# Kernel optimization log

Hardware: AMD Instinct MI355X
Metric: run time of the kernel (lower is better)

Reference implementation:

```python
import jax, jax.numpy as jnp
import numpy as np

TOPK = 8
N_GROUPS = 8
TOPK_GROUPS = 4
ROUTE_SCALE = 2.5


def setup_inputs() -> dict:
    key = jax.random.key(0)
    k1, k2, k3 = jax.random.split(key, 3)
    T, D, E = 8192, 7168, 256
    x = jax.random.normal(k1, (T, D), dtype=jnp.float32)
    weight = jax.random.normal(k2, (E, D), dtype=jnp.float32) * 0.02
    bias = jax.random.normal(k3, (E,), dtype=jnp.float32) * 0.01
    return {"x": x, "weight": weight, "bias": bias}


def reference(x, weight, bias):
    T = x.shape[0]
    E = weight.shape[0]
    # gate GEMM in fp32 (x.float() @ weight.float().T) + sigmoid scoring
    scores = jax.nn.sigmoid(jnp.einsum('td,ed->te', x, weight))  # [T, E]
    original_scores = scores
    s = scores + bias  # bias only affects routing decisions, not weights
    # group-limited routing: [T, n_groups, experts_per_group]
    sg = s.reshape(T, N_GROUPS, E // N_GROUPS)
    # bias branch: group score = sum of top-2 expert scores within group
    group_scores = jax.lax.top_k(sg, 2)[0].sum(axis=-1)  # [T, G]
    gidx = jax.lax.top_k(group_scores, TOPK_GROUPS)[1]   # [T, topk_groups]
    keep = jnp.zeros((T, N_GROUPS), dtype=bool).at[
        jnp.arange(T)[:, None], gidx].set(True)
    masked = jnp.where(keep[:, :, None], sg, -jnp.inf).reshape(T, E)
    indices = jax.lax.top_k(masked, TOPK)[1]  # [T, topk]
    weights = jnp.take_along_axis(original_scores, indices, axis=1)
    weights = weights / weights.sum(axis=-1, keepdims=True)  # sigmoid norm
    weights = weights * ROUTE_SCALE
    return weights, indices
```

## Files before the change

### kernel.cpp

```cpp
#include <hip/hip_runtime.h>
#include <math.h>

#define T_TOK 8192
#define D_DIM 7168
#define E_EXP 256
#define TOPKN 8
#define NGRP 8
#define TOPG 4
#define ROUTE_SCALEF 2.5f

#define BM 128
#define BK 32

typedef _Float16 f16;
typedef f16 f16x8 __attribute__((ext_vector_type(8)));
typedef float f32x4 __attribute__((ext_vector_type(4)));

__global__ __launch_bounds__(256)
void split_w(const float* __restrict__ W, f16* __restrict__ Wh, f16* __restrict__ Wl) {
  const int e  = blockIdx.x;
  const int se = (e >> 1) & 3;
  for (int s = threadIdx.x; s < D_DIM / 8; s += 256) {
    const int t = s >> 2, c = s & 3;
    const int kin  = t * 32 + ((c ^ se) << 3);
    const int kout = t * 32 + (c << 3);
    const float4 v0 = *(const float4*)(W + (size_t)e * D_DIM + kin);
    const float4 v1 = *(const float4*)(W + (size_t)e * D_DIM + kin + 4);
    const float pe[8] = {v0.x, v0.y, v0.z, v0.w, v1.x, v1.y, v1.z, v1.w};
    f16x8 h, l;
#pragma unroll
    for (int m = 0; m < 8; ++m) {
      const float hf = (float)(f16)pe[m];
      h[m] = (f16)(hf * 64.0f);
      l[m] = (f16)((pe[m] - hf) * 64.0f);
    }
    *(f16x8*)(Wh + (size_t)e * D_DIM + kout) = h;
    *(f16x8*)(Wl + (size_t)e * D_DIM + kout) = l;
  }
}

__device__ __forceinline__ void gload_lds16(const void* g, void* l) {
  __builtin_amdgcn_global_load_lds(
      (const __attribute__((address_space(1))) unsigned int*)g,
      (__attribute__((address_space(3))) unsigned int*)l, 16, 0, 0);
}

__global__ __launch_bounds__(512, 4)
void gate_gemm(const float* __restrict__ X, const f16* __restrict__ Wh,
               const f16* __restrict__ Wl, float* __restrict__ partial, int kper) {
  __shared__ f16 Ah[BM][BK], Al[BM][BK];
  __shared__ f16 Bh[E_EXP][BK], Bl[E_EXP][BK];

  const int tid   = threadIdx.x;
  const int lane  = tid & 63;
  const int wid   = tid >> 6;
  const int mb    = blockIdx.x;
  const int ks    = blockIdx.y;
  const int kbase = ks * kper;
  const int ntile = kper >> 5;

  const int sr = wid * 16 + (lane & 15);
  const int sc = lane >> 4;
  const float* Xp = X + (size_t)(mb * BM + sr) * D_DIM + kbase + (sc << 3);
  const int awoff = ((sc ^ ((sr >> 1) & 3)) << 3);

  const f16* Whp = Wh + (size_t)(wid * 32 + (lane >> 2)) * D_DIM + kbase + ((lane & 3) << 3);
  const f16* Wlp = Wl + (size_t)(wid * 32 + (lane >> 2)) * D_DIM + kbase + ((lane & 3) << 3);

  const int wm0 = (wid >> 2) * 64;
  const int wn0 = (wid & 3) * 64;
  const int fr  = lane & 15;
  const int rdoff = (((lane >> 4) << 3)) ^ (((fr >> 1) & 3) << 3);

  f32x4 acc[4][4];
#pragma unroll
  for (int i = 0; i < 4; ++i)
#pragma unroll
    for (int j = 0; j < 4; ++j) acc[i][j] = f32x4{0.f, 0.f, 0.f, 0.f};

  float4 pa0 = *(const float4*)(Xp);
  float4 pa1 = *(const float4*)(Xp + 4);

#pragma unroll 1
  for (int kt = 0; kt < ntile; ++kt) {
    const int kc = kt << 5;

    gload_lds16(Whp + kc,                      &Bh[wid * 32][0]);
    gload_lds16(Whp + kc + (size_t)16 * D_DIM, &Bh[wid * 32 + 16][0]);
    gload_lds16(Wlp + kc,                      &Bl[wid * 32][0]);
    gload_lds16(Wlp + kc + (size_t)16 * D_DIM, &Bl[wid * 32 + 16][0]);

    const int knext = (kt + 1 < ntile) ? kc + 32 : kc;
    const float4 na0 = *(const float4*)(Xp + knext);
    const float4 na1 = *(const float4*)(Xp + knext + 4);

    const float pe[8] = {pa0.x, pa0.y, pa0.z, pa0.w, pa1.x, pa1.y, pa1.z, pa1.w};
    f16x8 hv, lv;
#pragma unroll
    for (int m = 0; m < 8; ++m) {
      const float hf = (float)(f16)pe[m];
      hv[m] = (f16)(hf * 64.0f);
      lv[m] = (f16)((pe[m] - hf) * 64.0f);
    }
    *(f16x8*)&Ah[sr][awoff] = hv;
    *(f16x8*)&Al[sr][awoff] = lv;
    pa0 = na0; pa1 = na1;

    __syncthreads();

    f16x8 bh0 = *(const f16x8*)&Bh[wn0 +  0 + fr][rdoff];
    f16x8 bl0 = *(const f16x8*)&Bl[wn0 +  0 + fr][rdoff];
    f16x8 bh1 = *(const f16x8*)&Bh[wn0 + 16 + fr][rdoff];
    f16x8 bl1 = *(const f16x8*)&Bl[wn0 + 16 + fr][rdoff];
    f16x8 bh2 = *(const f16x8*)&Bh[wn0 + 32 + fr][rdoff];
    f16x8 bl2 = *(const f16x8*)&Bl[wn0 + 32 + fr][rdoff];
    f16x8 bh3 = *(const f16x8*)&Bh[wn0 + 48 + fr][rdoff];
    f16x8 bl3 = *(const f16x8*)&Bl[wn0 + 48 + fr][rdoff];
#pragma unroll
    for (int i = 0; i < 4; ++i) {
      const f16x8 ah = *(const f16x8*)&Ah[wm0 + i * 16 + fr][rdoff];
      const f16x8 al = *(const f16x8*)&Al[wm0 + i * 16 + fr][rdoff];
      acc[i][0] = __builtin_amdgcn_mfma_f32_16x16x32_f16(ah, bh0, acc[i][0], 0, 0, 0);
      acc[i][0] = __builtin_amdgcn_mfma_f32_16x16x32_f16(ah, bl0, acc[i][0], 0, 0, 0);
      acc[i][0] = __builtin_amdgcn_mfma_f32_16x16x32_f16(al, bh0, acc[i][0], 0, 0, 0);
      acc[i][1] = __builtin_amdgcn_mfma_f32_16x16x32_f16(ah, bh1, acc[i][1], 0, 0, 0);
      acc[i][1] = __builtin_amdgcn_mfma_f32_16x16x32_f16(ah, bl1, acc[i][1], 0, 0, 0);
      acc[i][1] = __builtin_amdgcn_mfma_f32_16x16x32_f16(al, bh1, acc[i][1], 0, 0, 0);
      acc[i][2] = __builtin_amdgcn_mfma_f32_16x16x32_f16(ah, bh2, acc[i][2], 0, 0, 0);
      acc[i][2] = __builtin_amdgcn_mfma_f32_16x16x32_f16(ah, bl2, acc[i][2], 0, 0, 0);
      acc[i][2] = __builtin_amdgcn_mfma_f32_16x16x32_f16(al, bh2, acc[i][2], 0, 0, 0);
      acc[i][3] = __builtin_amdgcn_mfma_f32_16x16x32_f16(ah, bh3, acc[i][3], 0, 0, 0);
      acc[i][3] = __builtin_amdgcn_mfma_f32_16x16x32_f16(ah, bl3, acc[i][3], 0, 0, 0);
      acc[i][3] = __builtin_amdgcn_mfma_f32_16x16x32_f16(al, bh3, acc[i][3], 0, 0, 0);
    }
    __syncthreads();
  }

  const float s = 1.0f / 4096.0f;
  float* pout = partial + (size_t)ks * T_TOK * E_EXP;
#pragma unroll
  for (int i = 0; i < 4; ++i) {
    const int row0 = mb * BM + wm0 + i * 16 + (lane >> 4) * 4;
#pragma unroll
    for (int j = 0; j < 4; ++j) {
      const int col = wn0 + j * 16 + fr;
      const f32x4 v = acc[i][j] * s;
#pragma unroll
      for (int r = 0; r < 4; ++r)
        pout[(size_t)(row0 + r) * E_EXP + col] = v[r];
    }
  }
}

__global__ __launch_bounds__(256)
void gate_route(const float* __restrict__ partial, const float* __restrict__ bias,
                float* __restrict__ wout, float* __restrict__ iout, int ksplit) {
  const int t    = (blockIdx.x * 256 + threadIdx.x) >> 6;
  const int lane = threadIdx.x & 63;

  float sx = 0.f, sy = 0.f, sz = 0.f, sw = 0.f;
  for (int ks = 0; ks < ksplit; ++ks) {
    const float4 p = *(const float4*)(partial + ((size_t)ks * T_TOK + t) * E_EXP + (lane << 2));
    sx += p.x; sy += p.y; sz += p.z; sw += p.w;
  }
  const float o0 = 1.f / (1.f + expf(-sx));
  const float o1 = 1.f / (1.f + expf(-sy));
  const float o2 = 1.f / (1.f + expf(-sz));
  const float o3 = 1.f / (1.f + expf(-sw));
  const float4 bv4 = *(const float4*)(bias + (lane << 2));
  const float b0 = o0 + bv4.x, b1 = o1 + bv4.y, b2 = o2 + bv4.z, b3 = o3 + bv4.w;

  const float ma = fmaxf(b0, b1), mi = fminf(b0, b1);
  const float mb_ = fmaxf(b2, b3), mn = fminf(b2, b3);
  float m1 = fmaxf(ma, mb_);
  float m2 = fmaxf(fminf(ma, mb_), fmaxf(mi, mn));
#pragma unroll
  for (int msk = 1; msk <= 4; msk <<= 1) {
    const float p1 = __shfl_xor(m1, msk);
    const float p2 = __shfl_xor(m2, msk);
    const float nm1 = fmaxf(m1, p1);
    const float nm2 = fmaxf(fminf(m1, p1), fmaxf(m2, p2));
    m1 = nm1; m2 = nm2;
  }
  const float gs = m1 + m2;

  float ga[8];
#pragma unroll
  for (int g = 0; g < 8; ++g) ga[g] = __shfl(gs, g * 8);
  int keepmask = 0;
#pragma unroll
  for (int r = 0; r < TOPG; ++r) {
    float bvv = -INFINITY; int bg = 0;
#pragma unroll
    for (int g = 0; g < NGRP; ++g) {
      const bool better = !((keepmask >> g) & 1) && (ga[g] > bvv);
      bvv = better ? ga[g] : bvv;
      bg  = better ? g : bg;
    }
    keepmask |= 1 << bg;
  }

  const bool kept = (keepmask >> (lane >> 3)) & 1;
  const float c0 = kept ? b0 : -INFINITY;
  const float c1 = kept ? b1 : -INFINITY;
  const float c2 = kept ? b2 : -INFINITY;
  const float c3 = kept ? b3 : -INFINITY;

  int used = 0;
  float sum = 0.f, selw = 0.f;
  int seli = 0;
#pragma unroll
  for (int r = 0; r < TOPKN; ++r) {
    float bv_ = -INFINITY; int bi_ = 0x7FFFFFFF; float bo_ = 0.f;
    { const bool ok = !(used & 1) && (c0 > bv_); bv_ = ok ? c0 : bv_; bi_ = ok ? (lane << 2)     : bi_; bo_ = ok ? o0 : bo_; }
    { const bool ok = !(used & 2) && (c1 > bv_); bv_ = ok ? c1 : bv_; bi_ = ok ? (lane << 2) | 1 : bi_; bo_ = ok ? o1 : bo_; }
    { const bool ok = !(used & 4) && (c2 > bv_); bv_ = ok ? c2 : bv_; bi_ = ok ? (lane << 2) | 2 : bi_; bo_ = ok ? o2 : bo_; }
    { const bool ok = !(used & 8) && (c3 > bv_); bv_ = ok ? c3 : bv_; bi_ = ok ? (lane << 2) | 3 : bi_; bo_ = ok ? o3 : bo_; }
#pragma unroll
    for (int m = 1; m < 64; m <<= 1) {
      const float vp = __shfl_xor(bv_, m);
      const int   ip = __shfl_xor(bi_, m);
      const float op = __shfl_xor(bo_, m);
      const bool take = (vp > bv_) || (vp == bv_ && ip < bi_);
      bv_ = take ? vp : bv_; bi_ = take ? ip : bi_; bo_ = take ? op : bo_;
    }
    sum += bo_;
    if (lane == r) { selw = bo_; seli = bi_; }
    if ((bi_ >> 2) == lane) used |= 1 << (bi_ & 3);
  }

  if (lane < TOPKN) {
    wout[(size_t)t * TOPKN + lane] = (selw / sum) * ROUTE_SCALEF;
    iout[(size_t)t * TOPKN + lane] = (float)seli;
  }
}

extern "C" void kernel_launch(void* const* d_in, const int* in_sizes, int n_in,
                              void* d_out, int out_size, void* d_ws, size_t ws_size,
                              hipStream_t stream) {
  const float* x = (const float*)d_in[0];
  const float* w = (const float*)d_in[1];
  const float* b = (const float*)d_in[2];
  float* out = (float*)d_out;

  const size_t whl = (size_t)E_EXP * D_DIM * sizeof(f16);
  const size_t per_split = (size_t)T_TOK * E_EXP * sizeof(float);
  const int ksplit = (ws_size >= 2 * whl + 8 * per_split) ? 8 : 4;

  f16* Wh = (f16*)d_ws;
  f16* Wl = Wh + (size_t)E_EXP * D_DIM;
  float* partial = (float*)(Wl + (size_t)E_EXP * D_DIM);

  split_w<<<E_EXP, 256, 0, stream>>>(w, Wh, Wl);

  dim3 gg(T_TOK / BM, ksplit);
  gate_gemm<<<gg, 512, 0, stream>>>(x, Wh, Wl, partial, D_DIM / ksplit);

  float* wout = out;
  float* iout = out + (size_t)T_TOK * TOPKN;
  gate_route<<<T_TOK / 4, 256, 0, stream>>>(partial, b, wout, iout, ksplit);
}
```

Before: 412.4 us.

## Double-buffer W tiles in LDS and feed X fragments from registers

The gate GEMM now keeps the W tiles in two LDS buffers, so the next tile's global-to-LDS load overlaps MFMA work on the current tile. This cuts one barrier per tile. X is no longer staged through LDS: each wave loads its own rows, splits them into fp16 hi/lo in registers and uses them directly as MFMA operands. The warp tiling changes to 32x128 per wave, and the k-split is fixed at 8 with a flattened grid. The cost is higher register pressure (occupancy hint lowered to 2) and no fallback to a 4-way split when the workspace is small.

```diff
diff --git a/kernel.cpp b/kernel.cpp
--- a/kernel.cpp
+++ b/kernel.cpp
@@ -9,8 +9,11 @@
 #define TOPG 4
 #define ROUTE_SCALEF 2.5f
 
+#define KSPLIT 8
+#define KPER (D_DIM / KSPLIT)
+#define NTILE (KPER / 32)
 #define BM 128
-#define BK 32
+#define BN 256
 
 typedef _Float16 f16;
 typedef f16 f16x8 __attribute__((ext_vector_type(8)));
@@ -45,111 +48,107 @@
       (__attribute__((address_space(3))) unsigned int*)l, 16, 0, 0);
 }
 
-__global__ __launch_bounds__(512, 4)
+__device__ __forceinline__ void cvt8(const float4 a, const float4 b, f16x8& h, f16x8& l) {
+  const float pe[8] = {a.x, a.y, a.z, a.w, b.x, b.y, b.z, b.w};
+#pragma unroll
+  for (int m = 0; m < 8; ++m) {
+    const float hf = (float)(f16)pe[m];
+    h[m] = (f16)(hf * 64.0f);
+    l[m] = (f16)((pe[m] - hf) * 64.0f);
+  }
+}
+
+__global__ __launch_bounds__(512, 2)
 void gate_gemm(const float* __restrict__ X, const f16* __restrict__ Wh,
-               const f16* __restrict__ Wl, float* __restrict__ partial, int kper) {
-  __shared__ f16 Ah[BM][BK], Al[BM][BK];
-  __shared__ f16 Bh[E_EXP][BK], Bl[E_EXP][BK];
-
-  const int tid   = threadIdx.x;
-  const int lane  = tid & 63;
-  const int wid   = tid >> 6;
-  const int mb    = blockIdx.x;
-  const int ks    = blockIdx.y;
-  const int kbase = ks * kper;
-  const int ntile = kper >> 5;
-
-  const int sr = wid * 16 + (lane & 15);
-  const int sc = lane >> 4;
-  const float* Xp = X + (size_t)(mb * BM + sr) * D_DIM + kbase + (sc << 3);
-  const int awoff = ((sc ^ ((sr >> 1) & 3)) << 3);
-
-  const f16* Whp = Wh + (size_t)(wid * 32 + (lane >> 2)) * D_DIM + kbase + ((lane & 3) << 3);
-  const f16* Wlp = Wl + (size_t)(wid * 32 + (lane >> 2)) * D_DIM + kbase + ((lane & 3) << 3);
-
-  const int wm0 = (wid >> 2) * 64;
-  const int wn0 = (wid & 3) * 64;
+               const f16* __restrict__ Wl, float* __restrict__ partial) {
+  __shared__ f16 BhL[2][BN][32];
+  __shared__ f16 BlL[2][BN][32];
+
+  const int tid  = threadIdx.x;
+  const int lane = tid & 63;
+  const int wid  = tid >> 6;
+  const int mb = blockIdx.x >> 3, ks = blockIdx.x & 7;
+  const int kbase = ks * KPER;
+
+  const int wm = (wid >> 1) * 32;
+  const int wn = (wid & 1) * 128;
   const int fr  = lane & 15;
-  const int rdoff = (((lane >> 4) << 3)) ^ (((fr >> 1) & 3) << 3);
-
-  f32x4 acc[4][4];
-#pragma unroll
-  for (int i = 0; i < 4; ++i)
-#pragma unroll
-    for (int j = 0; j < 4; ++j) acc[i][j] = f32x4{0.f, 0.f, 0.f, 0.f};
-
-  float4 pa0 = *(const float4*)(Xp);
-  float4 pa1 = *(const float4*)(Xp + 4);
+  const int kch = lane >> 4;
+
+  const float* pA0 = X + (size_t)(mb * BM + wm + fr) * D_DIM + kbase + kch * 8;
+  const float* pA1 = pA0 + (size_t)16 * D_DIM;
+
+  const f16* sWh = Wh + (size_t)(wid * 32 + (lane >> 2)) * D_DIM + kbase + ((lane & 3) << 3);
+  const f16* sWl = Wl + (size_t)(wid * 32 + (lane >> 2)) * D_DIM + kbase + ((lane & 3) << 3);
+
+  const int rdoff = (kch << 3) ^ (((fr >> 1) & 3) << 3);
+
+  f32x4 acc[2][8];
+#pragma unroll
+  for (int i = 0; i < 2; ++i)
+#pragma unroll
+    for (int j = 0; j < 8; ++j) acc[i][j] = f32x4{0.f, 0.f, 0.f, 0.f};
+
+  float4 pc0 = *(const float4*)(pA0);
+  float4 pc1 = *(const float4*)(pA0 + 4);
+  float4 pc2 = *(const float4*)(pA1);
+  float4 pc3 = *(const float4*)(pA1 + 4);
+  gload_lds16(sWh,                      &BhL[0][wid * 32][0]);
+  gload_lds16(sWh + (size_t)16 * D_DIM, &BhL[0][wid * 32 + 16][0]);
+  gload_lds16(sWl,                      &BlL[0][wid * 32][0]);
+  gload_lds16(sWl + (size_t)16 * D_DIM, &BlL[0][wid * 32 + 16][0]);
+  float4 pn0, pn1, pn2, pn3;
+  __syncthreads();
+
+  auto phase = [&](int kcN, int bufC, int bufN,
+                   const float4& c0, const float4& c1, const float4& c2, const float4& c3,
+                   float4& n0, float4& n1, float4& n2, float4& n3) {
+    n0 = *(const float4*)(pA0 + kcN);
+    n1 = *(const float4*)(pA0 + kcN + 4);
+    n2 = *(const float4*)(pA1 + kcN);
+    n3 = *(const float4*)(pA1 + kcN + 4);
+    gload_lds16(sWh + kcN,                      &BhL[bufN][wid * 32][0]);
+    gload_lds16(sWh + kcN + (size_t)16 * D_DIM, &BhL[bufN][wid * 32 + 16][0]);
+    gload_lds16(sWl + kcN,                      &BlL[bufN][wid * 32][0]);
+    gload_lds16(sWl + kcN + (size_t)16 * D_DIM, &BlL[bufN][wid * 32 + 16][0]);
+    f16x8 ah0, al0, ah1, al1;
+    cvt8(c0, c1, ah0, al0);
+    cvt8(c2, c3, ah1, al1);
+#pragma unroll
+    for (int j = 0; j < 8; ++j) {
+      const f16x8 bh = *(const f16x8*)&BhL[bufC][wn + j * 16 + fr][rdoff];
+      const f16x8 bl = *(const f16x8*)&BlL[bufC][wn + j * 16 + fr][rdoff];
+      acc[0][j] = __builtin_amdgcn_mfma_f32_16x16x32_f16(ah0, bh, acc[0][j], 0, 0, 0);
+      acc[1][j] = __builtin_amdgcn_mfma_f32_16x16x32_f16(ah1, bh, acc[1][j], 0, 0, 0);
+      acc[0][j] = __builtin_amdgcn_mfma_f32_16x16x32_f16(ah0, bl, acc[0][j], 0, 0, 0);
+      acc[1][j] = __builtin_amdgcn_mfma_f32_16x16x32_f16(ah1, bl, acc[1][j], 0, 0, 0);
+      acc[0][j] = __builtin_amdgcn_mfma_f32_16x16x32_f16(al0, bh, acc[0][j], 0, 0, 0);
+      acc[1][j] = __builtin_amdgcn_mfma_f32_16x16x32_f16(al1, bh, acc[1][j], 0, 0, 0);
+    }
+    __syncthreads();
+  };
 
 #pragma unroll 1
-  for (int kt = 0; kt < ntile; ++kt) {
-    const int kc = kt << 5;
-
-    gload_lds16(Whp + kc,                      &Bh[wid * 32][0]);
-    gload_lds16(Whp + kc + (size_t)16 * D_DIM, &Bh[wid * 32 + 16][0]);
-    gload_lds16(Wlp + kc,                      &Bl[wid * 32][0]);
-    gload_lds16(Wlp + kc + (size_t)16 * D_DIM, &Bl[wid * 32 + 16][0]);
-
-    const int knext = (kt + 1 < ntile) ? kc + 32 : kc;
-    const float4 na0 = *(const float4*)(Xp + knext);
-    const float4 na1 = *(const float4*)(Xp + knext + 4);
-
-    const float pe[8] = {pa0.x, pa0.y, pa0.z, pa0.w, pa1.x, pa1.y, pa1.z, pa1.w};
-    f16x8 hv, lv;
-#pragma unroll
-    for (int m = 0; m < 8; ++m) {
-      const float hf = (float)(f16)pe[m];
-      hv[m] = (f16)(hf * 64.0f);
-      lv[m] = (f16)((pe[m] - hf) * 64.0f);
-    }
-    *(f16x8*)&Ah[sr][awoff] = hv;
-    *(f16x8*)&Al[sr][awoff] = lv;
-    pa0 = na0; pa1 = na1;
-
-    __syncthreads();
-
-    f16x8 bh0 = *(const f16x8*)&Bh[wn0 +  0 + fr][rdoff];
-    f16x8 bl0 = *(const f16x8*)&Bl[wn0 +  0 + fr][rdoff];
-    f16x8 bh1 = *(const f16x8*)&Bh[wn0 + 16 + fr][rdoff];
-    f16x8 bl1 = *(const f16x8*)&Bl[wn0 + 16 + fr][rdoff];
-    f16x8 bh2 = *(const f16x8*)&Bh[wn0 + 32 + fr][rdoff];
-    f16x8 bl2 = *(const f16x8*)&Bl[wn0 + 32 + fr][rdoff];
-    f16x8 bh3 = *(const f16x8*)&Bh[wn0 + 48 + fr][rdoff];
-    f16x8 bl3 = *(const f16x8*)&Bl[wn0 + 48 + fr][rdoff];
-#pragma unroll
-    for (int i = 0; i < 4; ++i) {
-      const f16x8 ah = *(const f16x8*)&Ah[wm0 + i * 16 + fr][rdoff];
-      const f16x8 al = *(const f16x8*)&Al[wm0 + i * 16 + fr][rdoff];
-      acc[i][0] = __builtin_amdgcn_mfma_f32_16x16x32_f16(ah, bh0, acc[i][0], 0, 0, 0);
-      acc[i][0] = __builtin_amdgcn_mfma_f32_16x16x32_f16(ah, bl0, acc[i][0], 0, 0, 0);
-      acc[i][0] = __builtin_amdgcn_mfma_f32_16x16x32_f16(al, bh0, acc[i][0], 0, 0, 0);
-      acc[i][1] = __builtin_amdgcn_mfma_f32_16x16x32_f16(ah, bh1, acc[i][1], 0, 0, 0);
-      acc[i][1] = __builtin_amdgcn_mfma_f32_16x16x32_f16(ah, bl1, acc[i][1], 0, 0, 0);
-      acc[i][1] = __builtin_amdgcn_mfma_f32_16x16x32_f16(al, bh1, acc[i][1], 0, 0, 0);
-      acc[i][2] = __builtin_amdgcn_mfma_f32_16x16x32_f16(ah, bh2, acc[i][2], 0, 0, 0);
-      acc[i][2] = __builtin_amdgcn_mfma_f32_16x16x32_f16(ah, bl2, acc[i][2], 0, 0, 0);
-      acc[i][2] = __builtin_amdgcn_mfma_f32_16x16x32_f16(al, bh2, acc[i][2], 0, 0, 0);
-      acc[i][3] = __builtin_amdgcn_mfma_f32_16x16x32_f16(ah, bh3, acc[i][3], 0, 0, 0);
-      acc[i][3] = __builtin_amdgcn_mfma_f32_16x16x32_f16(ah, bl3, acc[i][3], 0, 0, 0);
-      acc[i][3] = __builtin_amdgcn_mfma_f32_16x16x32_f16(al, bh3, acc[i][3], 0, 0, 0);
-    }
-    __syncthreads();
+  for (int kt = 0; kt < NTILE; kt += 2) {
+    const int kc1 = (kt + 1) * 32;
+    const int kc2 = ((kt + 2 < NTILE) ? (kt + 2) : (NTILE - 1)) * 32;
+    phase(kc1, 0, 1, pc0, pc1, pc2, pc3, pn0, pn1, pn2, pn3);
+    phase(kc2, 1, 0, pn0, pn1, pn2, pn3, pc0, pc1, pc2, pc3);
   }
 
   const float s = 1.0f / 4096.0f;
   float* pout = partial + (size_t)ks * T_TOK * E_EXP;
-#pragma unroll
-  for (int i = 0; i < 4; ++i) {
-    const int row0 = mb * BM + wm0 + i * 16 + (lane >> 4) * 4;
-#pragma unroll
-    for (int j = 0; j < 4; ++j) {
-      const int col = wn0 + j * 16 + fr;
+  const int orow = mb * BM + wm + (lane >> 4) * 4;
+  const int ocol = wn + fr;
+#pragma unroll
+  for (int i = 0; i < 2; ++i)
+#pragma unroll
+    for (int j = 0; j < 8; ++j) {
       const f32x4 v = acc[i][j] * s;
 #pragma unroll
       for (int r = 0; r < 4; ++r)
-        pout[(size_t)(row0 + r) * E_EXP + col] = v[r];
-    }
-  }
+        pout[(size_t)(orow + i * 16 + r) * E_EXP + ocol + j * 16] = v[r];
+    }
 }
 
 __global__ __launch_bounds__(256)
@@ -243,20 +242,15 @@
   const float* b = (const float*)d_in[2];
   float* out = (float*)d_out;
 
-  const size_t whl = (size_t)E_EXP * D_DIM * sizeof(f16);
-  const size_t per_split = (size_t)T_TOK * E_EXP * sizeof(float);
-  const int ksplit = (ws_size >= 2 * whl + 8 * per_split) ? 8 : 4;
-
   f16* Wh = (f16*)d_ws;
   f16* Wl = Wh + (size_t)E_EXP * D_DIM;
   float* partial = (float*)(Wl + (size_t)E_EXP * D_DIM);
 
   split_w<<<E_EXP, 256, 0, stream>>>(w, Wh, Wl);
 
-  dim3 gg(T_TOK / BM, ksplit);
-  gate_gemm<<<gg, 512, 0, stream>>>(x, Wh, Wl, partial, D_DIM / ksplit);
+  gate_gemm<<<(T_TOK / BM) * KSPLIT, 512, 0, stream>>>(x, Wh, Wl, partial);
 
   float* wout = out;
   float* iout = out + (size_t)T_TOK * TOPKN;
-  gate_route<<<T_TOK / 4, 256, 0, stream>>>(partial, b, wout, iout, ksplit);
-}
+  gate_route<<<T_TOK / 4, 256, 0, stream>>>(partial, b, wout, iout, KSPLIT);
+}
```

New measurement: 452.3 us. 1.1x slower.
